# Performance work log

Measured on AMD Instinct MI355X. Metric: run time of the kernel, lower is better.

Reference implementation:

```python
import jax, jax.numpy as jnp
import numpy as np
import math

L = 32            # one_side_length; seq_len = L*L = 1024
EMBED = 768
NDIM = 16
N_SSM = 768
DIRS = 4
K = DIRS * N_SSM  # kernel_dim = 3072
REPEAT = EMBED // N_SSM
SCALE = math.sqrt(1.0 / NDIM)


def _compute_kernel(A_angle, A_radius, B1p, B2p, C1p, C2p):
    # Polar-parameterized complex diagonal A's (4 transition coeffs), sigmoid B, raw C.
    ang = jax.nn.sigmoid(A_angle) * (2.0 * math.pi)
    rad = jax.nn.sigmoid(A_radius)
    A = (rad * jnp.cos(ang) + 1j * (rad * jnp.sin(ang))).astype(jnp.complex64)  # (4,K,NDIM)
    A1, A2, A3, A4 = A[0], A[1], A[2], A[3]
    sB1 = jax.nn.sigmoid(B1p); sB2 = jax.nn.sigmoid(B2p)
    B1 = (sB1[..., 0] + 1j * sB1[..., 1]).astype(jnp.complex64)   # (K,NDIM)
    B2 = (sB2[..., 0] + 1j * sB2[..., 1]).astype(jnp.complex64)
    C1 = (C1p[..., 0] + 1j * C1p[..., 1]).astype(jnp.complex64)
    C2 = (C2p[..., 0] + 1j * C2p[..., 1]).astype(jnp.complex64)

    zeros = jnp.zeros((L, K, NDIM), jnp.complex64)

    # 2-D SSM impulse response (same math the torch module precomputes via the
    # vandermonde / coefficient-table expansion):
    #   x_h[i,j] = A1 x_h[i,j-1] + A2 x_v[i,j-1] + B1 delta[i,j]
    #   x_v[i,j] = A3 x_h[i-1,j] + A4 x_v[i-1,j] + B2 delta[i,j]
    #   k[i,j]   = scale * Re(C1 . x_h[i,j] + C2 . x_v[i,j])
    def row_step(carry, i):
        xh_prev, xv_prev = carry                    # row i-1 states, (L,K,NDIM)
        first = (i == 0).astype(jnp.float32)
        xv = A3 * xh_prev + A4 * xv_prev            # vertical flow from row above
        xv = xv.at[0].add(first * B2)               # impulse at (0,0)
        h0 = (first * B1).astype(jnp.complex64)     # x_h[i,0]
        def col_step(h, v_left):
            h_new = A1 * h + A2 * v_left            # horizontal flow within the row
            return h_new, h_new
        _, xh_rest = jax.lax.scan(col_step, h0, xv[:-1])
        xh = jnp.concatenate([h0[None], xh_rest], axis=0)
        return (xh, xv), (xh, xv)

    (_, _), (XH, XV) = jax.lax.scan(row_step, (zeros, zeros), jnp.arange(L))
    # XH, XV: (L, L, K, NDIM) complex
    k = SCALE * (jnp.einsum('ijhn,hn->ijh', XH, C1) + jnp.einsum('ijhn,hn->ijh', XV, C2))
    # boundary corrections exactly as in the torch module
    k = k.at[0, :, :].multiply(2.0)
    k = k.at[:, 0, :].multiply(2.0)
    k = k.at[0, 0, :].divide(4.0)
    return k.real                                   # (L, L, K) float32


def _forward(x, A_angle, A_radius, B1p, B2p, C1p, C2p, omega):
    S, B, D = x.shape
    residual = x * omega
    k = _compute_kernel(A_angle, A_radius, B1p, B2p, C1p, C2p)
    k = jnp.transpose(k, (2, 0, 1))                 # (K, L, L)
    x4 = jnp.transpose(x, (1, 2, 0)).reshape(B, D, L, L)
    s2 = (2 * L, 2 * L)
    flips = [(), (-2,), (-1,), (-2, -1)]
    out = jnp.zeros((B, D, L, L), jnp.float32)
    for idx, fl in enumerate(flips):                # 4 scan directions via flips
        kk = jnp.tile(k[idx * N_SSM:(idx + 1) * N_SSM], (REPEAT, 1, 1))  # (D,L,L)
        xc = jnp.flip(x4, axis=fl) if fl else x4
        kf = jnp.fft.rfft2(kk, s=s2)
        xf = jnp.fft.rfft2(xc, s=s2)
        cur = jnp.fft.irfft2(xf * kf, s=s2)[..., :L, :L]
        out = out + (jnp.flip(cur, axis=fl) if fl else cur)
    out = jnp.transpose(out.reshape(B, D, S), (2, 0, 1))  # back to (S,B,D)
    return jax.nn.silu(out + residual)


def setup_inputs() -> dict:
    key = jax.random.key(0)
    ks = jax.random.split(key, 9)
    x = jax.random.normal(ks[0], (L * L, 16, EMBED), jnp.float32)
    A_angle = jax.random.uniform(ks[1], (4, K, NDIM), jnp.float32, 0.5, 3.0)
    A_radius = jax.random.uniform(ks[2], (4, K, NDIM), jnp.float32, 0.5, 3.0)
    B1p = 0.2 * jax.random.normal(ks[3], (K, NDIM, 2), jnp.float32)
    B2p = 0.2 * jax.random.normal(ks[4], (K, NDIM, 2), jnp.float32)
    C1p = jax.random.normal(ks[5], (K, NDIM, 2), jnp.float32)
    C2p = jax.random.normal(ks[6], (K, NDIM, 2), jnp.float32)
    omega = jax.random.normal(ks[7], (EMBED,), jnp.float32)
    return {"x": x, "A_angle": A_angle, "A_radius": A_radius, "B1p": B1p,
            "B2p": B2p, "C1p": C1p, "C2p": C2p, "omega": omega}


def reference(x, A_angle, A_radius, B1p, B2p, C1p, C2p, omega):
    return _forward(x, A_angle, A_radius, B1p, B2p, C1p, C2p, omega)
```

## Files before the change

### kernel.cpp

```cpp
#include <hip/hip_runtime.h>
#include <cmath>

#define TWO_PI 6.283185307179586476925f

typedef float f2 __attribute__((ext_vector_type(2)));

__device__ __forceinline__ float sigm(float v) { return 1.0f / (1.0f + __expf(-v)); }
__device__ __forceinline__ f2 mnegi(f2 v) { return (f2){v.y, -v.x}; }
__device__ __forceinline__ f2 mposi(f2 v) { return (f2){-v.y, v.x}; }
__device__ __forceinline__ f2 cmulf(f2 a, f2 b) {
    return (f2){a.x, a.x} * b + (f2){a.y, a.y} * mposi(b);
}

template<int CTRL>
__device__ __forceinline__ float dpp0(float v) {
    return __int_as_float(__builtin_amdgcn_update_dpp(
        0, __float_as_int(v), CTRL, 0xf, 0xf, true));
}
#define DPP_SHR1 0x111
#define DPP_SHR2 0x112
#define DPP_SHR4 0x114
#define DPP_ROR8 0x128

__device__ __forceinline__ float swz_xor16(float v) {
    return __int_as_float(__builtin_amdgcn_ds_swizzle(__float_as_int(v), 0x401F));
}

__device__ __forceinline__ int swz(int r, int c) {
    return (r << 6) | (c ^ ((r ^ (r << 3)) & 63));
}

__device__ __forceinline__ int gfidx(int o, int m, int c) {
    return o + (c << 3) + (m << 9);
}

template<bool INV, bool HALF, bool PRUNE>
__device__ __forceinline__ void dft8(f2* x) {
    const float RS = 0.70710678118654752440f;
    f2 t0, t1, t2, t3, t4, t5, t6, t7;
    if (HALF) {
        t0 = x[0]; t4 = x[0]; t1 = x[1]; t5 = x[1];
        t2 = x[2]; t6 = x[2]; t3 = x[3]; t7 = x[3];
    } else {
        t0 = x[0] + x[4]; t4 = x[0] - x[4];
        t1 = x[1] + x[5]; t5 = x[1] - x[5];
        t2 = x[2] + x[6]; t6 = x[2] - x[6];
        t3 = x[3] + x[7]; t7 = x[3] - x[7];
    }
    f2 t5w, t6w, t7w;
    if (!INV) {
        t5w = RS * (t5 + mnegi(t5));
        t6w = mnegi(t6);
        t7w = RS * (mnegi(t7) - t7);
    } else {
        t5w = RS * (t5 - mnegi(t5));
        t6w = mposi(t6);
        t7w = RS * (mposi(t7) - t7);
    }
    f2 u0 = t0 + t2, u2 = t0 - t2, u1 = t1 + t3, dd = t1 - t3;
    f2 u3 = INV ? mposi(dd) : mnegi(dd);
    x[0] = u0 + u1; x[2] = u2 + u3;
    if (!PRUNE) { x[4] = u0 - u1; x[6] = u2 - u3; }
    f2 v0 = t4 + t6w, v2 = t4 - t6w, v1 = t5w + t7w, ee = t5w - t7w;
    f2 v3 = INV ? mposi(ee) : mnegi(ee);
    x[1] = v0 + v1; x[3] = v2 + v3;
    if (!PRUNE) { x[5] = v0 - v1; x[7] = v2 - v3; }
}

__device__ __forceinline__ void make_tw(int o, f2* tw) {
    float s, co;
    __sincosf(-TWO_PI * (float)o / 64.f, &s, &co);
    tw[0] = (f2){co, s};
#pragma unroll
    for (int k = 1; k < 7; ++k) tw[k] = cmulf(tw[k - 1], tw[0]);
}

template<bool INV, bool COL, bool HALF, bool PRUNE>
__device__ __forceinline__ void fft64(f2* a, f2* r, const f2* tw,
                                      int o, int line) {
    dft8<INV, HALF, false>(r);
#pragma unroll
    for (int k = 1; k < 8; ++k) {
        f2 w = tw[k - 1];
        if (INV) w.y = -w.y;
        r[k] = cmulf(r[k], w);
    }
#pragma unroll
    for (int m = 0; m < 8; ++m) {
        int s = 8 * o + m;
        a[COL ? swz(s, line) : swz(line, s)] = r[m];
    }
#pragma unroll
    for (int j = 0; j < 8; ++j) {
        int s = 8 * j + o;
        r[j] = a[COL ? swz(s, line) : swz(line, s)];
    }
    dft8<INV, false, PRUNE>(r);
}

__global__ __launch_bounds__(512) void ssm_tin(
        const float* __restrict__ Aang, const float* __restrict__ Arad,
        const float* __restrict__ B1p, const float* __restrict__ B2p,
        const float* __restrict__ C1p, const float* __restrict__ C2p,
        f2* __restrict__ Gf, const float* __restrict__ x,
        float* __restrict__ xT) {
    __shared__ __align__(16) char smem[35840];
    int tid = threadIdx.x;

    if (blockIdx.x >= 768) {
        float (*tt)[65] = (float (*)[65])smem;
        int bb = blockIdx.x - 768;
        int bR = bb % 192, bS = bb / 192;
        int r0 = bR * 64, s0 = bS * 64;
        int c = tid & 63, w = tid >> 6;
#pragma unroll
        for (int k = 0; k < 8; ++k) {
            int row = w + 8 * k;
            tt[row][c] = x[(size_t)(s0 + row) * 12288 + r0 + c];
        }
        __syncthreads();
#pragma unroll
        for (int k = 0; k < 8; ++k) {
            int row = w + 8 * k;
            xT[(size_t)(r0 + row) * 1024 + s0 + c] = tt[c][row];
        }
        return;
    }

    f2* a = (f2*)smem;
    float* row0 = (float*)(smem + 32768);
    float* col0 = (float*)(smem + 34816);
    int d = blockIdx.x;
    int w = tid >> 6;
    int t = w & 3;
    int nh = w >> 2;
    int lane = tid & 63;
    int jg = lane & 7;
    int n8 = lane >> 3;
    int n = n8 + 8 * nh;
    int ch = t * 768 + d;
    int gid = ch * 16 + n;

    for (int e = tid; e < 4096; e += 512) a[e] = (f2){0.f, 0.f};
    row0[tid] = 0.f;
    if (tid < 256) col0[tid] = 0.f;

    float ar[4], ai[4];
#pragma unroll
    for (int q = 0; q < 4; ++q) {
        float ang = sigm(Aang[q * 49152 + gid]) * TWO_PI;
        float rad = sigm(Arad[q * 49152 + gid]);
        float s, co;
        __sincosf(ang, &s, &co);
        ar[q] = rad * co; ai[q] = rad * s;
    }
    float a1r = ar[0], a1i = ai[0], a2r = ar[1], a2i = ai[1];
    float a3r = ar[2], a3i = ai[2], a4r = ar[3], a4i = ai[3];
    float p2r = a1r * a1r - a1i * a1i, p2i = 2.f * a1r * a1i;
    float p3r = a1r * p2r - a1i * p2i, p3i = a1r * p2i + a1i * p2r;
    float p4r = p2r * p2r - p2i * p2i, p4i = 2.f * p2r * p2i;
    float p8r = p4r * p4r - p4i * p4i, p8i = 2.f * p4r * p4i;
    float p16r = p8r * p8r - p8i * p8i, p16i = 2.f * p8r * p8i;
    float cz1r = (jg >= 1) ? p4r : 0.f,  cz1i = (jg >= 1) ? p4i : 0.f;
    float cz2r = (jg >= 2) ? p8r : 0.f,  cz2i = (jg >= 2) ? p8i : 0.f;
    float cz4r = (jg >= 4) ? p16r : 0.f, cz4i = (jg >= 4) ? p16i : 0.f;

    const float2* B1v = (const float2*)B1p;
    const float2* B2v = (const float2*)B2p;
    const float2* C1v = (const float2*)C1p;
    const float2* C2v = (const float2*)C2p;
    float2 b1 = B1v[gid], b2 = B2v[gid], c1 = C1v[gid], c2 = C2v[gid];
    float b1r = sigm(b1.x), b1i = sigm(b1.y);
    float b2r = sigm(b2.x), b2i = sigm(b2.y);
    float c1r = c1.x, c1i = c1.y, c2r = c2.x, c2i = c2.y;

    float pwr = 1.f, pwi = 0.f;
    if (jg & 1) { pwr = p4r; pwi = p4i; }
    if (jg & 2) { float tr = pwr * p8r - pwi * p8i;  pwi = pwr * p8i + pwi * p8r;  pwr = tr; }
    if (jg & 4) { float tr = pwr * p16r - pwi * p16i; pwi = pwr * p16i + pwi * p16r; pwr = tr; }
    float ebr = pwr * b1r - pwi * b1i, ebi = pwr * b1i + pwi * b1r;

    int bb0 = n8 & 1, bb1 = (n8 >> 1) & 1;
    int col = 4 * jg + 2 * bb0 + bb1;
    int ccl = (t & 2) ? ((64 - col) & 63) : col;

    __syncthreads();

    float xvr[4], xvi[4], xhr[4], xhi[4];
#pragma unroll
    for (int m = 0; m < 4; ++m) { xvr[m] = 0.f; xvi[m] = 0.f; xhr[m] = 0.f; xhi[m] = 0.f; }

    auto body = [&](int i, bool is0) {
#pragma unroll
        for (int m = 0; m < 4; ++m) {
            float nr = a3r * xhr[m] - a3i * xhi[m] + a4r * xvr[m] - a4i * xvi[m];
            float ni = a3r * xhi[m] + a3i * xhr[m] + a4r * xvi[m] + a4i * xvr[m];
            xvr[m] = nr; xvi[m] = ni;
        }
        if (is0 && jg == 0) { xvr[0] += b2r; xvi[0] += b2i; }
        float g1r = a2r * xvr[0] - a2i * xvi[0];
        float g1i = a2r * xvi[0] + a2i * xvr[0];
        float g2r = a1r * g1r - a1i * g1i + a2r * xvr[1] - a2i * xvi[1];
        float g2i = a1r * g1i + a1i * g1r + a2r * xvi[1] + a2i * xvr[1];
        float g3r = a1r * g2r - a1i * g2i + a2r * xvr[2] - a2i * xvi[2];
        float g3i = a1r * g2i + a1i * g2r + a2r * xvi[2] + a2i * xvr[2];
        float ldr = a1r * g3r - a1i * g3i + a2r * xvr[3] - a2i * xvi[3];
        float ldi = a1r * g3i + a1i * g3r + a2r * xvi[3] + a2i * xvr[3];
        float Vr = ldr, Vi = ldi, sr, si;
        sr = dpp0<DPP_SHR1>(Vr); si = dpp0<DPP_SHR1>(Vi);
        Vr += cz1r * sr - cz1i * si; Vi += cz1r * si + cz1i * sr;
        sr = dpp0<DPP_SHR2>(Vr); si = dpp0<DPP_SHR2>(Vi);
        Vr += cz2r * sr - cz2i * si; Vi += cz2r * si + cz2i * sr;
        sr = dpp0<DPP_SHR4>(Vr); si = dpp0<DPP_SHR4>(Vi);
        Vr += cz4r * sr - cz4i * si; Vi += cz4r * si + cz4i * sr;
        float Er = dpp0<DPP_SHR1>(Vr), Ei = dpp0<DPP_SHR1>(Vi);
        Er = (jg == 0) ? 0.f : Er; Ei = (jg == 0) ? 0.f : Ei;
        if (is0) { Er += ebr; Ei += ebi; }
        xhr[0] = Er; xhi[0] = Ei;
        xhr[1] = a1r * Er - a1i * Ei + g1r;  xhi[1] = a1r * Ei + a1i * Er + g1i;
        xhr[2] = p2r * Er - p2i * Ei + g2r;  xhi[2] = p2r * Ei + p2i * Er + g2i;
        xhr[3] = p3r * Er - p3i * Ei + g3r;  xhi[3] = p3r * Ei + p3i * Er + g3i;
        float v0 = c1r * xhr[0] - c1i * xhi[0] + c2r * xvr[0] - c2i * xvi[0];
        float v1 = c1r * xhr[1] - c1i * xhi[1] + c2r * xvr[1] - c2i * xvi[1];
        float v2 = c1r * xhr[2] - c1i * xhi[2] + c2r * xvr[2] - c2i * xvi[2];
        float v3 = c1r * xhr[3] - c1i * xhi[3] + c2r * xvr[3] - c2i * xvi[3];
        float s0 = bb0 ? v0 : v2, s1 = bb0 ? v1 : v3;
        float r0 = dpp0<DPP_ROR8>(s0), r1 = dpp0<DPP_ROR8>(s1);
        float q0 = (bb0 ? v2 : v0) + r0;
        float q1 = (bb0 ? v3 : v1) + r1;
        float s2 = bb1 ? q0 : q1;
        float r2 = swz_xor16(s2);
        float qq = (bb1 ? q1 : q0) + r2;
        qq += __shfl_xor(qq, 32, 64);
        if (n8 < 4) {
            if (is0) {
                row0[(((t << 1) | nh) << 6) | ccl] = qq;
            } else if (col == 0) {
                col0[((((t >> 1) << 1) | nh) << 6) | ((t & 1) ? (64 - i) : i)] = qq;
            } else {
                int rr_ = (t & 1) ? (64 - i) : i;
                ((float*)&a[swz(rr_, ccl)])[nh] = qq;
            }
        }
    };
    body(0, true);
#pragma unroll 1
    for (int i = 1; i < 32; ++i) body(i, false);

    __syncthreads();
    for (int e = tid; e < 4096; e += 512) {
        int r = e >> 6, cm = e & 63;
        int c = cm ^ ((r ^ (r << 3)) & 63);
        f2 cv = a[e];
        float v = cv.x + cv.y;
        if (r == 0) {
            v += row0[c] + row0[64 + c] + row0[128 + c] + row0[192 + c]
               + row0[256 + c] + row0[320 + c] + row0[384 + c] + row0[448 + c];
        } else if (c == 0) {
            v += col0[r] + col0[64 + r] + col0[128 + r] + col0[192 + r];
        }
        float f = 0.25f;
        if (r == 0) f *= 2.f;
        if (c == 0) f *= 2.f;
        if (r == 0 && c == 0) f *= 0.25f;
        a[e] = (f2){f * v, 0.f};
    }
    __syncthreads();
    int o = tid & 7;
    f2 tw[7];
    make_tw(o, tw);
    {
        int row = tid >> 3;
        f2 r[8];
#pragma unroll
        for (int j = 0; j < 8; ++j) r[j] = a[swz(row, 8 * j + o)];
        fft64<false, false, false, false>(a, r, tw, o, row);
#pragma unroll
        for (int m = 0; m < 8; ++m) a[swz(row, o + 8 * m)] = r[m];
    }
    __syncthreads();
    {
        int cc = tid >> 3;
        f2 r[8];
#pragma unroll
        for (int j = 0; j < 8; ++j) r[j] = a[swz(8 * j + o, cc)];
        fft64<false, true, false, false>(a, r, tw, o, cc);
#pragma unroll
        for (int m = 0; m < 8; ++m) Gf[d * 4096 + gfidx(o, m, cc)] = r[m];
    }
}

__global__ __launch_bounds__(512) void conv_fft(
        const float* __restrict__ x, float* __restrict__ xT,
        const f2* __restrict__ Gf, const float* __restrict__ omega,
        float* __restrict__ out, int useT) {
    __shared__ f2 a[4096];
    int bid = (blockIdx.x & 7) * 768 + (blockIdx.x >> 3);
    int d = bid >> 3, b = (bid & 7) * 2;
    int tid = threadIdx.x;
    int o = tid & 7, grp = tid >> 3;
    f2 tw[7];
    make_tw(o, tw);
    const size_t base0 = (size_t)(b * 768 + d) * 1024;
    const size_t base1 = (size_t)((b + 1) * 768 + d) * 1024;
    if (grp < 32) {
        int row = grp;
        f2 r[8];
#pragma unroll
        for (int j = 0; j < 4; ++j) {
            int s2 = row * 32 + 8 * j + o;
            if (useT) r[j] = (f2){xT[base0 + s2], xT[base1 + s2]};
            else      r[j] = (f2){x[s2 * 12288 + b * 768 + d],
                                  x[s2 * 12288 + (b + 1) * 768 + d]};
        }
#pragma unroll
        for (int j = 4; j < 8; ++j) r[j] = (f2){0.f, 0.f};
        fft64<false, false, true, false>(a, r, tw, o, row);
#pragma unroll
        for (int m = 0; m < 8; ++m) a[swz(row, o + 8 * m)] = r[m];
    }
    __syncthreads();
    {
        int c = grp;
        f2 r[8];
#pragma unroll
        for (int j = 0; j < 4; ++j) r[j] = a[swz(8 * j + o, c)];
#pragma unroll
        for (int j = 4; j < 8; ++j) r[j] = (f2){0.f, 0.f};
        fft64<false, true, true, false>(a, r, tw, o, c);
#pragma unroll
        for (int m = 0; m < 8; ++m) {
            r[m] = cmulf(r[m], Gf[d * 4096 + gfidx(o, m, c)]);
        }
        fft64<true, true, false, true>(a, r, tw, o, c);
#pragma unroll
        for (int m = 0; m < 4; ++m) a[swz(o + 8 * m, c)] = r[m];
    }
    __syncthreads();
    if (grp < 32) {
        int row = grp;
        f2 r[8];
#pragma unroll
        for (int j = 0; j < 8; ++j) r[j] = a[swz(row, 8 * j + o)];
        fft64<true, false, false, true>(a, r, tw, o, row);
        float w = omega[d];
        const float inv = 1.0f / 4096.0f;
#pragma unroll
        for (int m = 0; m < 4; ++m) {
            int cc = o + 8 * m;
            int s2 = row * 32 + cc;
            float xa, xb;
            if (useT) { xa = xT[base0 + s2]; xb = xT[base1 + s2]; }
            else {
                xa = x[s2 * 12288 + b * 768 + d];
                xb = x[s2 * 12288 + (b + 1) * 768 + d];
            }
            float ya = r[m].x * inv + xa * w;
            float yb = r[m].y * inv + xb * w;
            float oa = ya / (1.0f + __expf(-ya));
            float ob = yb / (1.0f + __expf(-yb));
            if (useT) {
                xT[base0 + s2] = oa;
                xT[base1 + s2] = ob;
            } else {
                out[s2 * 12288 + b * 768 + d] = oa;
                out[s2 * 12288 + (b + 1) * 768 + d] = ob;
            }
        }
    }
}

__global__ __launch_bounds__(256) void transpose_out(const float* __restrict__ xT,
                                                     float* __restrict__ out) {
    __shared__ float t[64][65];
    int bR = blockIdx.x % 192, bS = blockIdx.x / 192;
    int r0 = bR * 64, s0 = bS * 64;
    int c = threadIdx.x & 63, w = threadIdx.x >> 6;
#pragma unroll
    for (int k = 0; k < 16; ++k) {
        int row = w + 4 * k;
        t[row][c] = xT[(size_t)(r0 + row) * 1024 + s0 + c];
    }
    __syncthreads();
#pragma unroll
    for (int k = 0; k < 16; ++k) {
        int row = w + 4 * k;
        out[(size_t)(s0 + row) * 12288 + r0 + c] = t[c][row];
    }
}

extern "C" void kernel_launch(void* const* d_in, const int* in_sizes, int n_in,
                              void* d_out, int out_size, void* d_ws, size_t ws_size,
                              hipStream_t stream) {
    const float* x     = (const float*)d_in[0];
    const float* Aang  = (const float*)d_in[1];
    const float* Arad  = (const float*)d_in[2];
    const float* B1p   = (const float*)d_in[3];
    const float* B2p   = (const float*)d_in[4];
    const float* C1p   = (const float*)d_in[5];
    const float* C2p   = (const float*)d_in[6];
    const float* omega = (const float*)d_in[7];
    float* out = (float*)d_out;
    char* ws = (char*)d_ws;

    f2*    Gf = (f2*)ws;
    float* xT = (float*)(ws + 25165824);
    int useT = (ws_size >= (size_t)75497472) ? 1 : 0;

    int grid1 = useT ? 3840 : 768;
    ssm_tin<<<grid1, 512, 0, stream>>>(Aang, Arad, B1p, B2p, C1p, C2p, Gf, x, xT);
    conv_fft<<<6144, 512, 0, stream>>>(x, xT, Gf, omega, out, useT);
    if (useT) transpose_out<<<3072, 256, 0, stream>>>(xT, out);
}
```

Before: 153.7 us.

## Process two batch-pair tiles per conv block and vectorize SSM complex math

The conv_fft kernel now handles four batch channels per block, as two 64x64 tiles in doubled shared memory. All 512 threads now do row FFTs in the first and last phases, where previously only half were active, and the column phase loops over both tiles. The grid is halved. Separately, the SSM scan code is rewritten using packed float2 complex ops (cms, dpp2), which may let the compiler emit packed FMA instructions. The doubled LDS footprint (64KB) may reduce occupancy.

```diff
diff --git a/kernel.cpp b/kernel.cpp
--- a/kernel.cpp
+++ b/kernel.cpp
@@ -11,11 +11,18 @@
 __device__ __forceinline__ f2 cmulf(f2 a, f2 b) {
     return (f2){a.x, a.x} * b + (f2){a.y, a.y} * mposi(b);
 }
+__device__ __forceinline__ f2 cms(f2 A, f2 v) {
+    return (f2){A.x, A.x} * v + (f2){A.y, A.y} * (f2){-v.y, v.x};
+}
 
 template<int CTRL>
 __device__ __forceinline__ float dpp0(float v) {
     return __int_as_float(__builtin_amdgcn_update_dpp(
         0, __float_as_int(v), CTRL, 0xf, 0xf, true));
+}
+template<int CTRL>
+__device__ __forceinline__ f2 dpp2(f2 v) {
+    return (f2){dpp0<CTRL>(v.x), dpp0<CTRL>(v.y)};
 }
 #define DPP_SHR1 0x111
 #define DPP_SHR2 0x112
@@ -145,40 +152,39 @@
     row0[tid] = 0.f;
     if (tid < 256) col0[tid] = 0.f;
 
-    float ar[4], ai[4];
+    f2 A[4];
 #pragma unroll
     for (int q = 0; q < 4; ++q) {
         float ang = sigm(Aang[q * 49152 + gid]) * TWO_PI;
         float rad = sigm(Arad[q * 49152 + gid]);
         float s, co;
         __sincosf(ang, &s, &co);
-        ar[q] = rad * co; ai[q] = rad * s;
-    }
-    float a1r = ar[0], a1i = ai[0], a2r = ar[1], a2i = ai[1];
-    float a3r = ar[2], a3i = ai[2], a4r = ar[3], a4i = ai[3];
-    float p2r = a1r * a1r - a1i * a1i, p2i = 2.f * a1r * a1i;
-    float p3r = a1r * p2r - a1i * p2i, p3i = a1r * p2i + a1i * p2r;
-    float p4r = p2r * p2r - p2i * p2i, p4i = 2.f * p2r * p2i;
-    float p8r = p4r * p4r - p4i * p4i, p8i = 2.f * p4r * p4i;
-    float p16r = p8r * p8r - p8i * p8i, p16i = 2.f * p8r * p8i;
-    float cz1r = (jg >= 1) ? p4r : 0.f,  cz1i = (jg >= 1) ? p4i : 0.f;
-    float cz2r = (jg >= 2) ? p8r : 0.f,  cz2i = (jg >= 2) ? p8i : 0.f;
-    float cz4r = (jg >= 4) ? p16r : 0.f, cz4i = (jg >= 4) ? p16i : 0.f;
+        A[q] = (f2){rad * co, rad * s};
+    }
+    f2 A1 = A[0], A2 = A[1], A3 = A[2], A4 = A[3];
+    f2 P2 = cms(A1, A1);
+    f2 P3 = cms(A1, P2);
+    f2 P4 = cms(P2, P2);
+    f2 P8 = cms(P4, P4);
+    f2 P16 = cms(P8, P8);
+    f2 CZ1 = (jg >= 1) ? P4 : (f2){0.f, 0.f};
+    f2 CZ2 = (jg >= 2) ? P8 : (f2){0.f, 0.f};
+    f2 CZ4 = (jg >= 4) ? P16 : (f2){0.f, 0.f};
 
     const float2* B1v = (const float2*)B1p;
     const float2* B2v = (const float2*)B2p;
     const float2* C1v = (const float2*)C1p;
     const float2* C2v = (const float2*)C2p;
     float2 b1 = B1v[gid], b2 = B2v[gid], c1 = C1v[gid], c2 = C2v[gid];
-    float b1r = sigm(b1.x), b1i = sigm(b1.y);
-    float b2r = sigm(b2.x), b2i = sigm(b2.y);
+    f2 B1 = (f2){sigm(b1.x), sigm(b1.y)};
+    f2 B2 = (f2){sigm(b2.x), sigm(b2.y)};
     float c1r = c1.x, c1i = c1.y, c2r = c2.x, c2i = c2.y;
 
-    float pwr = 1.f, pwi = 0.f;
-    if (jg & 1) { pwr = p4r; pwi = p4i; }
-    if (jg & 2) { float tr = pwr * p8r - pwi * p8i;  pwi = pwr * p8i + pwi * p8r;  pwr = tr; }
-    if (jg & 4) { float tr = pwr * p16r - pwi * p16i; pwi = pwr * p16i + pwi * p16r; pwr = tr; }
-    float ebr = pwr * b1r - pwi * b1i, ebi = pwr * b1i + pwi * b1r;
+    f2 pw = (f2){1.f, 0.f};
+    if (jg & 1) pw = P4;
+    if (jg & 2) pw = cms(pw, P8);
+    if (jg & 4) pw = cms(pw, P16);
+    f2 EB = cms(pw, B1);
 
     int bb0 = n8 & 1, bb1 = (n8 >> 1) & 1;
     int col = 4 * jg + 2 * bb0 + bb1;
@@ -186,44 +192,32 @@
 
     __syncthreads();
 
-    float xvr[4], xvi[4], xhr[4], xhi[4];
-#pragma unroll
-    for (int m = 0; m < 4; ++m) { xvr[m] = 0.f; xvi[m] = 0.f; xhr[m] = 0.f; xhi[m] = 0.f; }
+    f2 xv[4], xh[4];
+#pragma unroll
+    for (int m = 0; m < 4; ++m) { xv[m] = (f2){0.f, 0.f}; xh[m] = (f2){0.f, 0.f}; }
 
     auto body = [&](int i, bool is0) {
 #pragma unroll
-        for (int m = 0; m < 4; ++m) {
-            float nr = a3r * xhr[m] - a3i * xhi[m] + a4r * xvr[m] - a4i * xvi[m];
-            float ni = a3r * xhi[m] + a3i * xhr[m] + a4r * xvi[m] + a4i * xvr[m];
-            xvr[m] = nr; xvi[m] = ni;
-        }
-        if (is0 && jg == 0) { xvr[0] += b2r; xvi[0] += b2i; }
-        float g1r = a2r * xvr[0] - a2i * xvi[0];
-        float g1i = a2r * xvi[0] + a2i * xvr[0];
-        float g2r = a1r * g1r - a1i * g1i + a2r * xvr[1] - a2i * xvi[1];
-        float g2i = a1r * g1i + a1i * g1r + a2r * xvi[1] + a2i * xvr[1];
-        float g3r = a1r * g2r - a1i * g2i + a2r * xvr[2] - a2i * xvi[2];
-        float g3i = a1r * g2i + a1i * g2r + a2r * xvi[2] + a2i * xvr[2];
-        float ldr = a1r * g3r - a1i * g3i + a2r * xvr[3] - a2i * xvi[3];
-        float ldi = a1r * g3i + a1i * g3r + a2r * xvi[3] + a2i * xvr[3];
-        float Vr = ldr, Vi = ldi, sr, si;
-        sr = dpp0<DPP_SHR1>(Vr); si = dpp0<DPP_SHR1>(Vi);
-        Vr += cz1r * sr - cz1i * si; Vi += cz1r * si + cz1i * sr;
-        sr = dpp0<DPP_SHR2>(Vr); si = dpp0<DPP_SHR2>(Vi);
-        Vr += cz2r * sr - cz2i * si; Vi += cz2r * si + cz2i * sr;
-        sr = dpp0<DPP_SHR4>(Vr); si = dpp0<DPP_SHR4>(Vi);
-        Vr += cz4r * sr - cz4i * si; Vi += cz4r * si + cz4i * sr;
-        float Er = dpp0<DPP_SHR1>(Vr), Ei = dpp0<DPP_SHR1>(Vi);
-        Er = (jg == 0) ? 0.f : Er; Ei = (jg == 0) ? 0.f : Ei;
-        if (is0) { Er += ebr; Ei += ebi; }
-        xhr[0] = Er; xhi[0] = Ei;
-        xhr[1] = a1r * Er - a1i * Ei + g1r;  xhi[1] = a1r * Ei + a1i * Er + g1i;
-        xhr[2] = p2r * Er - p2i * Ei + g2r;  xhi[2] = p2r * Ei + p2i * Er + g2i;
-        xhr[3] = p3r * Er - p3i * Ei + g3r;  xhi[3] = p3r * Ei + p3i * Er + g3i;
-        float v0 = c1r * xhr[0] - c1i * xhi[0] + c2r * xvr[0] - c2i * xvi[0];
-        float v1 = c1r * xhr[1] - c1i * xhi[1] + c2r * xvr[1] - c2i * xvi[1];
-        float v2 = c1r * xhr[2] - c1i * xhi[2] + c2r * xvr[2] - c2i * xvi[2];
-        float v3 = c1r * xhr[3] - c1i * xhi[3] + c2r * xvr[3] - c2i * xvi[3];
+        for (int m = 0; m < 4; ++m) xv[m] = cms(A3, xh[m]) + cms(A4, xv[m]);
+        if (is0 && jg == 0) xv[0] += B2;
+        f2 g1 = cms(A2, xv[0]);
+        f2 g2 = cms(A1, g1) + cms(A2, xv[1]);
+        f2 g3 = cms(A1, g2) + cms(A2, xv[2]);
+        f2 V  = cms(A1, g3) + cms(A2, xv[3]);
+        V += cms(CZ1, dpp2<DPP_SHR1>(V));
+        V += cms(CZ2, dpp2<DPP_SHR2>(V));
+        V += cms(CZ4, dpp2<DPP_SHR4>(V));
+        f2 E = dpp2<DPP_SHR1>(V);
+        if (jg == 0) E = (f2){0.f, 0.f};
+        if (is0) E += EB;
+        xh[0] = E;
+        xh[1] = cms(A1, E) + g1;
+        xh[2] = cms(P2, E) + g2;
+        xh[3] = cms(P3, E) + g3;
+        float v0 = c1r * xh[0].x - c1i * xh[0].y + c2r * xv[0].x - c2i * xv[0].y;
+        float v1 = c1r * xh[1].x - c1i * xh[1].y + c2r * xv[1].x - c2i * xv[1].y;
+        float v2 = c1r * xh[2].x - c1i * xh[2].y + c2r * xv[2].x - c2i * xv[2].y;
+        float v3 = c1r * xh[3].x - c1i * xh[3].y + c2r * xv[3].x - c2i * xv[3].y;
         float s0 = bb0 ? v0 : v2, s1 = bb0 ? v1 : v3;
         float r0 = dpp0<DPP_ROR8>(s0), r1 = dpp0<DPP_ROR8>(s1);
         float q0 = (bb0 ? v2 : v0) + r0;
@@ -294,55 +288,58 @@
         const float* __restrict__ x, float* __restrict__ xT,
         const f2* __restrict__ Gf, const float* __restrict__ omega,
         float* __restrict__ out, int useT) {
-    __shared__ f2 a[4096];
-    int bid = (blockIdx.x & 7) * 768 + (blockIdx.x >> 3);
-    int d = bid >> 3, b = (bid & 7) * 2;
+    __shared__ f2 a[8192];
+    int bid = (blockIdx.x & 7) * 384 + (blockIdx.x >> 3);
+    int d = bid >> 2, b0 = (bid & 3) * 4;
     int tid = threadIdx.x;
     int o = tid & 7, grp = tid >> 3;
+    int tl = grp >> 5, row = grp & 31;
     f2 tw[7];
     make_tw(o, tw);
-    const size_t base0 = (size_t)(b * 768 + d) * 1024;
-    const size_t base1 = (size_t)((b + 1) * 768 + d) * 1024;
-    if (grp < 32) {
-        int row = grp;
+    f2* at = a + (tl << 12);
+    int btl = b0 + 2 * tl;
+    const size_t base0 = (size_t)(btl * 768 + d) * 1024;
+    const size_t base1 = (size_t)((btl + 1) * 768 + d) * 1024;
+    {
         f2 r[8];
 #pragma unroll
         for (int j = 0; j < 4; ++j) {
             int s2 = row * 32 + 8 * j + o;
             if (useT) r[j] = (f2){xT[base0 + s2], xT[base1 + s2]};
-            else      r[j] = (f2){x[s2 * 12288 + b * 768 + d],
-                                  x[s2 * 12288 + (b + 1) * 768 + d]};
+            else      r[j] = (f2){x[s2 * 12288 + btl * 768 + d],
+                                  x[s2 * 12288 + (btl + 1) * 768 + d]};
         }
 #pragma unroll
         for (int j = 4; j < 8; ++j) r[j] = (f2){0.f, 0.f};
-        fft64<false, false, true, false>(a, r, tw, o, row);
-#pragma unroll
-        for (int m = 0; m < 8; ++m) a[swz(row, o + 8 * m)] = r[m];
-    }
-    __syncthreads();
-    {
+        fft64<false, false, true, false>(at, r, tw, o, row);
+#pragma unroll
+        for (int m = 0; m < 8; ++m) at[swz(row, o + 8 * m)] = r[m];
+    }
+    __syncthreads();
+#pragma unroll 1
+    for (int sw = 0; sw < 2; ++sw) {
+        f2* ac = a + (sw << 12);
         int c = grp;
         f2 r[8];
 #pragma unroll
-        for (int j = 0; j < 4; ++j) r[j] = a[swz(8 * j + o, c)];
+        for (int j = 0; j < 4; ++j) r[j] = ac[swz(8 * j + o, c)];
 #pragma unroll
         for (int j = 4; j < 8; ++j) r[j] = (f2){0.f, 0.f};
-        fft64<false, true, true, false>(a, r, tw, o, c);
+        fft64<false, true, true, false>(ac, r, tw, o, c);
 #pragma unroll
         for (int m = 0; m < 8; ++m) {
             r[m] = cmulf(r[m], Gf[d * 4096 + gfidx(o, m, c)]);
         }
-        fft64<true, true, false, true>(a, r, tw, o, c);
-#pragma unroll
-        for (int m = 0; m < 4; ++m) a[swz(o + 8 * m, c)] = r[m];
-    }
-    __syncthreads();
-    if (grp < 32) {
-        int row = grp;
+        fft64<true, true, false, true>(ac, r, tw, o, c);
+#pragma unroll
+        for (int m = 0; m < 4; ++m) ac[swz(o + 8 * m, c)] = r[m];
+    }
+    __syncthreads();
+    {
         f2 r[8];
 #pragma unroll
-        for (int j = 0; j < 8; ++j) r[j] = a[swz(row, 8 * j + o)];
-        fft64<true, false, false, true>(a, r, tw, o, row);
+        for (int j = 0; j < 8; ++j) r[j] = at[swz(row, 8 * j + o)];
+        fft64<true, false, false, true>(at, r, tw, o, row);
         float w = omega[d];
         const float inv = 1.0f / 4096.0f;
 #pragma unroll
@@ -352,8 +349,8 @@
             float xa, xb;
             if (useT) { xa = xT[base0 + s2]; xb = xT[base1 + s2]; }
             else {
-                xa = x[s2 * 12288 + b * 768 + d];
-                xb = x[s2 * 12288 + (b + 1) * 768 + d];
+                xa = x[s2 * 12288 + btl * 768 + d];
+                xb = x[s2 * 12288 + (btl + 1) * 768 + d];
             }
             float ya = r[m].x * inv + xa * w;
             float yb = r[m].y * inv + xb * w;
@@ -363,8 +360,8 @@
                 xT[base0 + s2] = oa;
                 xT[base1 + s2] = ob;
             } else {
-                out[s2 * 12288 + b * 768 + d] = oa;
-                out[s2 * 12288 + (b + 1) * 768 + d] = ob;
+                out[s2 * 12288 + btl * 768 + d] = oa;
+                out[s2 * 12288 + (btl + 1) * 768 + d] = ob;
             }
         }
     }
@@ -409,6 +406,6 @@
 
     int grid1 = useT ? 3840 : 768;
     ssm_tin<<<grid1, 512, 0, stream>>>(Aang, Arad, B1p, B2p, C1p, C2p, Gf, x, xT);
-    conv_fft<<<6144, 512, 0, stream>>>(x, xT, Gf, omega, out, useT);
+    conv_fft<<<3072, 512, 0, stream>>>(x, xT, Gf, omega, out, useT);
     if (useT) transpose_out<<<3072, 256, 0, stream>>>(xT, out);
 }
```

Result: slower. 170.9 us (+11.2%).
